# Performance work log

Hardware: AMD Instinct MI355X
Metric: run time of the kernel (lower is better)

## Reference

```python
import jax, jax.numpy as jnp
import numpy as np

H = 16
D_K = 64
D_V = 64


def setup_inputs() -> dict:
    key = jax.random.key(0)
    k0, k1, k2, k3, k4 = jax.random.split(key, 5)
    n, l, d_model = 4, 2048, 1024
    s = 1.0 / np.sqrt(d_model)
    Z = jax.random.normal(k0, (n, l, d_model), dtype=jnp.float32)
    mask = jnp.ones((n, 1, 1, l), dtype=jnp.int32)
    Wv = jax.random.normal(k1, (d_model, d_model), dtype=jnp.float32) * s
    Wk = jax.random.normal(k2, (d_model, H * D_K), dtype=jnp.float32) * s
    Wq = jax.random.normal(k3, (d_model, H * D_K), dtype=jnp.float32) * s
    Wo = jax.random.normal(k4, (H * D_V, d_model), dtype=jnp.float32) * s
    return {"Z": Z, "mask": mask, "Wv": Wv, "Wk": Wk, "Wq": Wq, "Wo": Wo}


def reference(Z, mask, Wv, Wk, Wq, Wo):
    n, l, d_model = Z.shape
    values = (Z @ Wv).reshape(n, l, H, D_V)
    keys = (Z @ Wk).reshape(n, l, H, D_K)
    queries = (Z @ Wq).reshape(n, l, H, D_K)
    # dense score matrix [n, h, q, k]
    C = jnp.einsum('nqhd,nkhd->nhqk', queries, keys)
    masked_C = jnp.where(mask == 0, -jnp.inf, C)
    idx = jnp.argmax(masked_C, axis=3)          # [n, h, q] hard top-1 index
    # torch einsum 'nhll,nlhd->nlhd' takes the diagonal of the one-hot
    # scattered C_tilde: diag element is C[n,h,l,l] iff argmax at query l is l.
    diag_C = jnp.einsum('nhll->nhl', C)         # [n, h, l]
    w = jnp.where(idx == jnp.arange(l)[None, None, :], diag_C, 0.0)  # [n, h, l]
    y_bar = (w.transpose(0, 2, 1)[..., None] * values).reshape(n, l, H * D_V)
    return y_bar @ Wo
```

## Files before the change

kernel.cpp:

```cpp
#include <hip/hip_runtime.h>
#include <hip/hip_bf16.h>
#include <string.h>

#define NB   4
#define LSEQ 2048
#define DMODEL 1024
#define NHEAD 16
#define DKH  64
#define CAND_CAP 32768

typedef __attribute__((ext_vector_type(8)))  short          short8v;
typedef __attribute__((ext_vector_type(8)))  unsigned short ushort8v;
typedef __attribute__((ext_vector_type(4)))  unsigned int   uint4v;
typedef __attribute__((ext_vector_type(16))) float          f32x16;

__device__ inline unsigned short bf16_rne(float v) {
  unsigned u = __builtin_bit_cast(unsigned, v);
  unsigned r = u + 0x7FFFu + ((u >> 16) & 1u);
  return (unsigned short)(r >> 16);
}
__device__ inline float bf16_to_f32(unsigned short u) {
  return __builtin_bit_cast(float, (unsigned)u << 16);
}
__device__ inline unsigned cvtpk2(float lo, float hi) {
  __hip_bfloat162 t = __float22bfloat162_rn(float2{lo, hi});
  unsigned u;
  memcpy(&u, &t, 4);
  return u;
}
__device__ inline void gload_lds16(const void* g, void* l) {
  __builtin_amdgcn_global_load_lds((const __attribute__((address_space(1))) void*)g,
                                   (__attribute__((address_space(3))) void*)l, 16, 0, 0);
}

__global__ __launch_bounds__(256) void zconv(
    const float* __restrict__ Z, unsigned short* __restrict__ Zbf) {
  size_t c = ((size_t)blockIdx.x * 256 + threadIdx.x) * 8;
  float4 a = *(const float4*)(Z + c), b = *(const float4*)(Z + c + 4);
  uint4v uv;
  uv[0] = cvtpk2(a.x, a.y);
  uv[1] = cvtpk2(a.z, a.w);
  uv[2] = cvtpk2(b.x, b.y);
  uv[3] = cvtpk2(b.z, b.w);
  *(ushort8v*)(Zbf + c) = __builtin_bit_cast(ushort8v, uv);
}

__global__ __launch_bounds__(256) void wconv(
    const float* __restrict__ Wq, const float* __restrict__ Wk,
    unsigned short* __restrict__ WThi) {
  __shared__ float T[64][65];
  const int col0 = blockIdx.x * 64, k0 = blockIdx.y * 64;
  const float* W = (col0 < 1024) ? Wq : Wk;
  const int cl0 = (col0 < 1024) ? col0 : col0 - 1024;
  const int tid = threadIdx.x;
#pragma unroll
  for (int u = 0; u < 16; ++u) {
    int lin = u * 256 + tid;
    int r = lin >> 6, c = lin & 63;
    T[r][c] = W[(size_t)(k0 + r) * 1024 + cl0 + c];
  }
  __syncthreads();
#pragma unroll
  for (int u = 0; u < 16; ++u) {
    int lin = u * 256 + tid;
    int cc = lin >> 6, kk = lin & 63;
    WThi[(size_t)(col0 + cc) * 1024 + k0 + kk] = bf16_rne(T[kk][cc]);
  }
}

__global__ __launch_bounds__(256) void proj_hi(
    const unsigned short* __restrict__ Zbf, const unsigned short* __restrict__ WThi,
    unsigned short* __restrict__ Qhd, unsigned short* __restrict__ Khd) {
  __shared__ unsigned short As[128 * 32];
  __shared__ unsigned short Bs[128 * 32];
  const int tid = threadIdx.x;
  const int lane = tid & 63, w = tid >> 6;
  const int l31 = lane & 31, half = lane >> 5;
  const int wrow = w >> 1, wcol = w & 1;
  const int bid = blockIdx.x;
  const int xcd = bid & 7, t = bid >> 3;
  const int brow = (xcd * 8 + (t & 7)) * 128;
  const int bcol = (t >> 3) * 128;

  int aoff[2], boff[2];
#pragma unroll
  for (int u = 0; u < 2; ++u) {
    int c = u * 256 + w * 64 + lane;
    int r = c >> 2, sp = c & 3;
    int s = sp ^ ((r >> 1) & 3);
    aoff[u] = (brow + r) * 1024 + s * 8;
    boff[u] = (bcol + r) * 1024 + s * 8;
  }

  f32x16 acc[2][2];
#pragma unroll
  for (int m = 0; m < 2; ++m)
#pragma unroll
    for (int nf = 0; nf < 2; ++nf)
#pragma unroll
      for (int r = 0; r < 16; ++r) acc[m][nf][r] = 0.f;

  for (int k0 = 0; k0 < 1024; k0 += 32) {
    __syncthreads();
#pragma unroll
    for (int u = 0; u < 2; ++u) {
      gload_lds16(Zbf  + (size_t)(aoff[u] + k0), (char*)As + u * 4096 + w * 1024);
      gload_lds16(WThi + (size_t)(boff[u] + k0), (char*)Bs + u * 4096 + w * 1024);
    }
    __syncthreads();
    short8v aH[2][2], bH[2][2];
#pragma unroll
    for (int m = 0; m < 2; ++m) {
      int r = wrow * 64 + m * 32 + l31;
      int sw = (r >> 1) & 3;
#pragma unroll
      for (int kc = 0; kc < 2; ++kc) {
        int sl = (kc * 2 + half) ^ sw;
        aH[m][kc] = *(const short8v*)((const char*)As + r * 64 + sl * 16);
      }
    }
#pragma unroll
    for (int nf = 0; nf < 2; ++nf) {
      int r = wcol * 64 + nf * 32 + l31;
      int sw = (r >> 1) & 3;
#pragma unroll
      for (int kc = 0; kc < 2; ++kc) {
        int sl = (kc * 2 + half) ^ sw;
        bH[nf][kc] = *(const short8v*)((const char*)Bs + r * 64 + sl * 16);
      }
    }
#pragma unroll
    for (int m = 0; m < 2; ++m)
#pragma unroll
      for (int nf = 0; nf < 2; ++nf)
#pragma unroll
        for (int kc = 0; kc < 2; ++kc)
          acc[m][nf] = __builtin_amdgcn_mfma_f32_32x32x16_bf16(aH[m][kc], bH[nf][kc], acc[m][nf], 0, 0, 0);
  }

  unsigned short* Out;
  int coff;
  if (bcol < 1024) { Out = Qhd; coff = bcol; } else { Out = Khd; coff = bcol - 1024; }
#pragma unroll
  for (int m = 0; m < 2; ++m)
#pragma unroll
    for (int nf = 0; nf < 2; ++nf) {
      int colg = coff + wcol * 64 + nf * 32 + l31;
      int head = colg >> 6, cin = colg & 63;
#pragma unroll
      for (int r = 0; r < 16; ++r) {
        int rowg = brow + wrow * 64 + m * 32 + (r & 3) + 8 * (r >> 2) + 4 * half;
        int n = rowg >> 11, l = rowg & 2047;
        Out[((size_t)(n * 16 + head) * 2048 + l) * 64 + cin] = bf16_rne(acc[m][nf][r]);
      }
    }
}

__global__ __launch_bounds__(256) void score_hi(
    const unsigned short* __restrict__ Qhd, const unsigned short* __restrict__ Khd,
    int* __restrict__ cnt_cand, int* __restrict__ cand) {
  __shared__ unsigned short Ks[64 * 128];
  const int tid = threadIdx.x;
  const int lane = tid & 63, w = tid >> 6;
  const int l31 = lane & 31, half = lane >> 5;
  const int bid = blockIdx.x;
  const int xcd = bid & 7, j = bid >> 3;
  const int nh = xcd + 8 * (j >> 4);
  const int qi = j & 15;
  const int n = nh >> 4, h = nh & 15;
  const int qw = qi * 128 + w * 32;

  const unsigned short* qrow = Qhd + ((size_t)(nh) * 2048 + qw + l31) * 64;
  short8v aQ[4];
#pragma unroll
  for (int ds = 0; ds < 4; ++ds)
    aQ[ds] = *(const short8v*)(qrow + ds * 16 + 8 * half);

  f32x16 zac;
#pragma unroll
  for (int r = 0; r < 16; ++r) zac[r] = 0.f;

  float maxO[16], diag[16];
#pragma unroll
  for (int r = 0; r < 16; ++r) { maxO[r] = -3.0e38f; diag[r] = -3.0e38f; }

  const unsigned short* kb = Khd + (size_t)nh * 2048 * 64;
  int koff[4];
#pragma unroll
  for (int u = 0; u < 4; ++u) {
    int c = u * 256 + w * 64 + lane;
    int pr = c >> 4, sp = c & 15;
    int ls = sp ^ (pr & 15);
    koff[u] = (2 * pr + (ls >> 3)) * 64 + (ls & 7) * 8;
  }

  for (int kt = 0; kt < LSEQ; kt += 128) {
    __syncthreads();
#pragma unroll
    for (int u = 0; u < 4; ++u)
      gload_lds16(kb + (size_t)kt * 64 + koff[u], (char*)Ks + u * 4096 + w * 1024);
    __syncthreads();
    char* buf = (char*)Ks;
    if (kt == qi * 128) {
#pragma unroll
      for (int ct = 0; ct < 4; ++ct) {
        const int rr = ct * 32 + l31;
        const int pr = rr >> 1;
        short8v bh[4];
#pragma unroll
        for (int ds = 0; ds < 4; ++ds) {
          int sl = ((rr & 1) << 3) | (2 * ds + half);
          bh[ds] = *(const short8v*)(buf + pr * 256 + ((sl ^ (pr & 15)) << 4));
        }
        f32x16 acc = __builtin_amdgcn_mfma_f32_32x32x16_bf16(aQ[0], bh[0], zac, 0, 0, 0);
#pragma unroll
        for (int ds = 1; ds < 4; ++ds)
          acc = __builtin_amdgcn_mfma_f32_32x32x16_bf16(aQ[ds], bh[ds], acc, 0, 0, 0);
        if (ct == w) {
#pragma unroll
          for (int r = 0; r < 16; ++r) {
            const int rloc = (r & 3) + 8 * (r >> 2) + 4 * half;
            if (l31 == rloc) diag[r] = acc[r];
            else             maxO[r] = fmaxf(maxO[r], acc[r]);
          }
        } else {
#pragma unroll
          for (int r = 0; r < 16; ++r) maxO[r] = fmaxf(maxO[r], acc[r]);
        }
      }
    } else {
#pragma unroll
      for (int p = 0; p < 2; ++p) {
        const int rrA = (2 * p) * 32 + l31, rrB = (2 * p + 1) * 32 + l31;
        const int prA = rrA >> 1, prB = rrB >> 1;
        short8v bA[4], bB[4];
#pragma unroll
        for (int ds = 0; ds < 4; ++ds) {
          int slA = ((rrA & 1) << 3) | (2 * ds + half);
          int slB = ((rrB & 1) << 3) | (2 * ds + half);
          bA[ds] = *(const short8v*)(buf + prA * 256 + ((slA ^ (prA & 15)) << 4));
          bB[ds] = *(const short8v*)(buf + prB * 256 + ((slB ^ (prB & 15)) << 4));
        }
        f32x16 accA = __builtin_amdgcn_mfma_f32_32x32x16_bf16(aQ[0], bA[0], zac, 0, 0, 0);
        f32x16 accB = __builtin_amdgcn_mfma_f32_32x32x16_bf16(aQ[0], bB[0], zac, 0, 0, 0);
#pragma unroll
        for (int ds = 1; ds < 4; ++ds) {
          accA = __builtin_amdgcn_mfma_f32_32x32x16_bf16(aQ[ds], bA[ds], accA, 0, 0, 0);
          accB = __builtin_amdgcn_mfma_f32_32x32x16_bf16(aQ[ds], bB[ds], accB, 0, 0, 0);
        }
#pragma unroll
        for (int r = 0; r < 16; ++r)
          maxO[r] = fmaxf(fmaxf(accA[r], accB[r]), maxO[r]);
      }
    }
  }

#pragma unroll
  for (int r = 0; r < 16; ++r) {
    float mo = maxO[r], dg = diag[r];
#pragma unroll
    for (int off = 16; off >= 1; off >>= 1) {
      mo = fmaxf(mo, __shfl_xor(mo, off));
      dg = fmaxf(dg, __shfl_xor(dg, off));
    }
    if (l31 == 0) {
      if (dg >= mo - 0.8f) {
        const int q = qw + (r & 3) + 8 * (r >> 2) + 4 * half;
        int slot = atomicAdd(cnt_cand, 1);
        if (slot < CAND_CAP) cand[slot] = (n << 15) | (h << 11) | q;
      }
    }
  }
}

__global__ __launch_bounds__(256) void recheck2(
    const float* __restrict__ Z, const float* __restrict__ Wq,
    const float* __restrict__ Wk, const float* __restrict__ Wv,
    const float* __restrict__ Wo, const unsigned short* __restrict__ Khd,
    const int* __restrict__ cnt_cand, const int* __restrict__ cand,
    float* __restrict__ out) {
  __shared__ float Zs[1024];
  __shared__ float part[4][64];
  __shared__ float Qex[64];
  __shared__ float Kex[64];
  __shared__ float Svals[2048];
  __shared__ float red[4];
  __shared__ int   Elist[64];
  __shared__ int   Ecnt;
  const int tid = threadIdx.x;
  const int lane = tid & 63, w = tid >> 6;
  int nc = *cnt_cand; if (nc > CAND_CAP) nc = CAND_CAP;

  for (int e = blockIdx.x; e < nc; e += gridDim.x) {
    const int pk = cand[e];
    const int n = pk >> 15, h = (pk >> 11) & 15, q = pk & 2047;
    __syncthreads();
#pragma unroll
    for (int u = 0; u < 4; ++u)
      Zs[tid + u * 256] = Z[((size_t)(n * LSEQ + q)) * 1024 + tid + u * 256];
    if (tid == 0) Ecnt = 0;
    __syncthreads();
    {
      int o = tid & 63, seg = tid >> 6;
      float p = 0.f;
      int d0 = seg * 256;
      for (int d = d0; d < d0 + 256; ++d) p += Zs[d] * Wq[(size_t)d * 1024 + h * 64 + o];
      part[seg][o] = p;
    }
    __syncthreads();
    if (tid < 64) Qex[tid] = part[0][tid] + part[1][tid] + part[2][tid] + part[3][tid];
    __syncthreads();
    const unsigned short* kb = Khd + (size_t)(n * 16 + h) * 2048 * 64;
    float mymax = -3.0e38f;
    for (int k = tid; k < LSEQ; k += 256) {
      const unsigned short* kr = kb + (size_t)k * 64;
      float s = 0.f;
#pragma unroll
      for (int jj = 0; jj < 8; ++jj) {
        ushort8v v = *(const ushort8v*)(kr + jj * 8);
#pragma unroll
        for (int ee = 0; ee < 8; ++ee) s += Qex[jj * 8 + ee] * bf16_to_f32(v[ee]);
      }
      Svals[k] = s;
      if (k != q) mymax = fmaxf(mymax, s);
    }
#pragma unroll
    for (int off = 32; off >= 1; off >>= 1) mymax = fmaxf(mymax, __shfl_xor(mymax, off));
    if (lane == 0) red[w] = mymax;
    __syncthreads();
    const float Mt = fmaxf(fmaxf(red[0], red[1]), fmaxf(red[2], red[3]));
    const float Sqt = Svals[q];
    if (Sqt < Mt - 0.4f) continue;
    for (int k = tid; k < LSEQ; k += 256) {
      if (k != q && Svals[k] >= Sqt - 0.4f) {
        int sl = atomicAdd(&Ecnt, 1);
        if (sl < 64) Elist[sl] = k;
      }
    }
    __syncthreads();
    const int nE = (Ecnt < 64) ? Ecnt : 64;
    float Sq_ex = 0.f;
    bool ok = true;
    for (int i = 0; i <= nE; ++i) {
      const int kk = (i == 0) ? q : Elist[i - 1];
      __syncthreads();
#pragma unroll
      for (int u = 0; u < 4; ++u)
        Zs[tid + u * 256] = Z[((size_t)(n * LSEQ + kk)) * 1024 + tid + u * 256];
      __syncthreads();
      {
        int o = tid & 63, seg = tid >> 6;
        float p = 0.f;
        int d0 = seg * 256;
        for (int d = d0; d < d0 + 256; ++d) p += Zs[d] * Wk[(size_t)d * 1024 + h * 64 + o];
        part[seg][o] = p;
      }
      __syncthreads();
      if (tid < 64) Kex[tid] = part[0][tid] + part[1][tid] + part[2][tid] + part[3][tid];
      __syncthreads();
      if (w == 0) {
        float pr = Qex[lane] * Kex[lane];
#pragma unroll
        for (int off = 32; off >= 1; off >>= 1) pr += __shfl_xor(pr, off);
        if (lane == 0) red[0] = pr;
      }
      __syncthreads();
      const float Sk = red[0];
      if (i == 0) Sq_ex = Sk;
      else        ok = ok && (kk < q ? (Sk < Sq_ex) : (Sk <= Sq_ex));
      __syncthreads();
    }
    if (!ok) continue;
    __syncthreads();
#pragma unroll
    for (int u = 0; u < 4; ++u)
      Zs[tid + u * 256] = Z[((size_t)(n * LSEQ + q)) * 1024 + tid + u * 256];
    __syncthreads();
    {
      int o = tid & 63, seg = tid >> 6;
      float p = 0.f;
      int d0 = seg * 256;
      for (int d = d0; d < d0 + 256; ++d) p += Zs[d] * Wv[(size_t)d * 1024 + h * 64 + o];
      part[seg][o] = p;
    }
    __syncthreads();
    if (tid < 64) Kex[tid] = part[0][tid] + part[1][tid] + part[2][tid] + part[3][tid];
    __syncthreads();
    {
      float a4[4] = {0.f, 0.f, 0.f, 0.f};
      const float* wo = Wo + (size_t)h * DKH * DMODEL;
      for (int jj = 0; jj < 64; ++jj) {
        float vj = Kex[jj];
#pragma unroll
        for (int u = 0; u < 4; ++u) a4[u] += vj * wo[(size_t)jj * DMODEL + tid + u * 256];
      }
      float* orow = out + ((size_t)n * LSEQ + q) * DMODEL;
#pragma unroll
      for (int u = 0; u < 4; ++u) atomicAdd(&orow[tid + u * 256], Sq_ex * a4[u]);
    }
  }
}

extern "C" void kernel_launch(void* const* d_in, const int* in_sizes, int n_in,
                              void* d_out, int out_size, void* d_ws, size_t ws_size,
                              hipStream_t stream) {
  const float* Z  = (const float*)d_in[0];
  const float* Wv = (const float*)d_in[2];
  const float* Wk = (const float*)d_in[3];
  const float* Wq = (const float*)d_in[4];
  const float* Wo = (const float*)d_in[5];
  float* out = (float*)d_out;

  int* cnt_cand = (int*)d_ws;
  int* cand = (int*)((char*)d_ws + 64);
  unsigned short* Khd  = (unsigned short*)((char*)d_ws + (size_t)(4 << 20));
  unsigned short* WThi = (unsigned short*)((char*)d_ws + (size_t)(24 << 20));
  unsigned short* Zbf  = (unsigned short*)((char*)d_ws + (size_t)(28 << 20));
  unsigned short* Qhd  = (unsigned short*)d_out;

  hipMemsetAsync(d_ws, 0, 64, stream);

  zconv<<<4096, 256, 0, stream>>>(Z, Zbf);

  dim3 gw(32, 16);
  wconv<<<gw, 256, 0, stream>>>(Wq, Wk, WThi);

  proj_hi<<<1024, 256, 0, stream>>>(Zbf, WThi, Qhd, Khd);

  score_hi<<<1024, 256, 0, stream>>>(Qhd, Khd, cnt_cand, cand);

  hipMemsetAsync(d_out, 0, (size_t)out_size * sizeof(float), stream);
  recheck2<<<256, 256, 0, stream>>>(Z, Wq, Wk, Wv, Wo, Khd, cnt_cand, cand, out);
}
```

Baseline: 186.4 us.

## Recheck scores via precomputed Wk·q vector instead of per-candidate key projections

In the exact recheck stage, the per-head query is folded into a 1024-wide vector u = Wk_h·q, computed once from a transposed fp32 copy of Wk. Each competing key's score then becomes a single dot product of its Z row with u, evaluated in parallel with one wave per candidate and an early exit on the first failure. Previously every competitor needed a full 1024x64 key projection in sequence. The change also adds a transpose kernel for Wk, splits the Q and V projections into four partial accumulators, doubles the recheck grid, and compacts the workspace layout. Associating the product differently can shift fp32 rounding in tie-sensitive comparisons.

```diff
diff --git a/kernel.cpp b/kernel.cpp
--- a/kernel.cpp
+++ b/kernel.cpp
@@ -65,6 +65,26 @@
     int lin = u * 256 + tid;
     int cc = lin >> 6, kk = lin & 63;
     WThi[(size_t)(col0 + cc) * 1024 + k0 + kk] = bf16_rne(T[kk][cc]);
+  }
+}
+
+__global__ __launch_bounds__(256) void wtr(
+    const float* __restrict__ Wk, float* __restrict__ WkT) {
+  __shared__ float T[64][65];
+  const int c0 = blockIdx.x * 64, d0 = blockIdx.y * 64;
+  const int tid = threadIdx.x;
+#pragma unroll
+  for (int u = 0; u < 16; ++u) {
+    int lin = u * 256 + tid;
+    int r = lin >> 6, c = lin & 63;
+    T[r][c] = Wk[(size_t)(d0 + r) * 1024 + c0 + c];
+  }
+  __syncthreads();
+#pragma unroll
+  for (int u = 0; u < 16; ++u) {
+    int lin = u * 256 + tid;
+    int cc = lin >> 6, dd = lin & 63;
+    WkT[(size_t)(c0 + cc) * 1024 + d0 + dd] = T[dd][cc];
   }
 }
 
@@ -273,22 +293,27 @@
   }
 }
 
-__global__ __launch_bounds__(256) void recheck2(
+__global__ __launch_bounds__(256) void recheck3(
     const float* __restrict__ Z, const float* __restrict__ Wq,
-    const float* __restrict__ Wk, const float* __restrict__ Wv,
-    const float* __restrict__ Wo, const unsigned short* __restrict__ Khd,
+    const float* __restrict__ Wv, const float* __restrict__ Wo,
+    const float* __restrict__ WkT, const unsigned short* __restrict__ Khd,
     const int* __restrict__ cnt_cand, const int* __restrict__ cand,
     float* __restrict__ out) {
   __shared__ float Zs[1024];
+  __shared__ float Us[1024];
   __shared__ float part[4][64];
   __shared__ float Qex[64];
   __shared__ float Kex[64];
   __shared__ float Svals[2048];
   __shared__ float red[4];
+  __shared__ float Sband[4];
+  __shared__ float SqS;
   __shared__ int   Elist[64];
   __shared__ int   Ecnt;
+  __shared__ int   okf;
   const int tid = threadIdx.x;
   const int lane = tid & 63, w = tid >> 6;
+  const int o = tid & 63, seg = tid >> 6;
   int nc = *cnt_cand; if (nc > CAND_CAP) nc = CAND_CAP;
 
   for (int e = blockIdx.x; e < nc; e += gridDim.x) {
@@ -298,17 +323,47 @@
 #pragma unroll
     for (int u = 0; u < 4; ++u)
       Zs[tid + u * 256] = Z[((size_t)(n * LSEQ + q)) * 1024 + tid + u * 256];
-    if (tid == 0) Ecnt = 0;
+    if (tid == 0) { Ecnt = 0; okf = 1; }
     __syncthreads();
     {
-      int o = tid & 63, seg = tid >> 6;
-      float p = 0.f;
+      const float* wc = Wq + h * 64 + o;
       int d0 = seg * 256;
-      for (int d = d0; d < d0 + 256; ++d) p += Zs[d] * Wq[(size_t)d * 1024 + h * 64 + o];
-      part[seg][o] = p;
+      float p0 = 0.f, p1 = 0.f, p2 = 0.f, p3 = 0.f;
+#pragma unroll
+      for (int d = 0; d < 256; d += 4) {
+        p0 += Zs[d0 + d]     * wc[(size_t)(d0 + d) * 1024];
+        p1 += Zs[d0 + d + 1] * wc[(size_t)(d0 + d + 1) * 1024];
+        p2 += Zs[d0 + d + 2] * wc[(size_t)(d0 + d + 2) * 1024];
+        p3 += Zs[d0 + d + 3] * wc[(size_t)(d0 + d + 3) * 1024];
+      }
+      part[seg][o] = (p0 + p1) + (p2 + p3);
     }
     __syncthreads();
     if (tid < 64) Qex[tid] = part[0][tid] + part[1][tid] + part[2][tid] + part[3][tid];
+    __syncthreads();
+    {
+      float u0 = 0.f, u1 = 0.f, u2 = 0.f, u3 = 0.f;
+      const float* base = WkT + (size_t)(h * 64) * 1024 + tid;
+      for (int c = 0; c < 64; ++c) {
+        float qc = Qex[c];
+        const float* col = base + (size_t)c * 1024;
+        u0 += qc * col[0];
+        u1 += qc * col[256];
+        u2 += qc * col[512];
+        u3 += qc * col[768];
+      }
+      Us[tid] = u0; Us[tid + 256] = u1; Us[tid + 512] = u2; Us[tid + 768] = u3;
+    }
+    __syncthreads();
+    {
+      float p = Zs[tid] * Us[tid] + Zs[tid + 256] * Us[tid + 256]
+              + Zs[tid + 512] * Us[tid + 512] + Zs[tid + 768] * Us[tid + 768];
+#pragma unroll
+      for (int off = 32; off >= 1; off >>= 1) p += __shfl_xor(p, off);
+      if (lane == 0) red[w] = p;
+    }
+    __syncthreads();
+    if (tid == 0) SqS = (red[0] + red[1]) + (red[2] + red[3]);
     __syncthreads();
     const unsigned short* kb = Khd + (size_t)(n * 16 + h) * 2048 * 64;
     float mymax = -3.0e38f;
@@ -339,49 +394,55 @@
     }
     __syncthreads();
     const int nE = (Ecnt < 64) ? Ecnt : 64;
-    float Sq_ex = 0.f;
-    bool ok = true;
-    for (int i = 0; i <= nE; ++i) {
-      const int kk = (i == 0) ? q : Elist[i - 1];
+    const float Sq_ex = SqS;
+    for (int i0 = 0; i0 < nE; i0 += 4) {
+      const int i = i0 + w;
+      float sk = 0.f;
+      if (i < nE) {
+        const int kk = Elist[i];
+        const float* zr = Z + ((size_t)(n * LSEQ + kk)) * 1024 + lane * 16;
+        float p0 = 0.f, p1 = 0.f;
+#pragma unroll
+        for (int jj = 0; jj < 16; jj += 8) {
+          float4 a = *(const float4*)(zr + jj);
+          float4 b = *(const float4*)(zr + jj + 4);
+          p0 += a.x * Us[lane * 16 + jj]     + a.y * Us[lane * 16 + jj + 1]
+              + a.z * Us[lane * 16 + jj + 2] + a.w * Us[lane * 16 + jj + 3];
+          p1 += b.x * Us[lane * 16 + jj + 4] + b.y * Us[lane * 16 + jj + 5]
+              + b.z * Us[lane * 16 + jj + 6] + b.w * Us[lane * 16 + jj + 7];
+        }
+        float p = p0 + p1;
+#pragma unroll
+        for (int off = 32; off >= 1; off >>= 1) p += __shfl_xor(p, off);
+        sk = p;
+      }
+      if (lane == 0) Sband[w] = sk;
       __syncthreads();
-#pragma unroll
-      for (int u = 0; u < 4; ++u)
-        Zs[tid + u * 256] = Z[((size_t)(n * LSEQ + kk)) * 1024 + tid + u * 256];
+      if (tid == 0) {
+        int okl = okf;
+        for (int ww = 0; ww < 4 && i0 + ww < nE; ++ww) {
+          int kk = Elist[i0 + ww];
+          float Sk = Sband[ww];
+          okl = okl && (kk < q ? (Sk < Sq_ex) : (Sk <= Sq_ex));
+        }
+        okf = okl;
+      }
       __syncthreads();
-      {
-        int o = tid & 63, seg = tid >> 6;
-        float p = 0.f;
-        int d0 = seg * 256;
-        for (int d = d0; d < d0 + 256; ++d) p += Zs[d] * Wk[(size_t)d * 1024 + h * 64 + o];
-        part[seg][o] = p;
-      }
-      __syncthreads();
-      if (tid < 64) Kex[tid] = part[0][tid] + part[1][tid] + part[2][tid] + part[3][tid];
-      __syncthreads();
-      if (w == 0) {
-        float pr = Qex[lane] * Kex[lane];
-#pragma unroll
-        for (int off = 32; off >= 1; off >>= 1) pr += __shfl_xor(pr, off);
-        if (lane == 0) red[0] = pr;
-      }
-      __syncthreads();
-      const float Sk = red[0];
-      if (i == 0) Sq_ex = Sk;
-      else        ok = ok && (kk < q ? (Sk < Sq_ex) : (Sk <= Sq_ex));
-      __syncthreads();
-    }
-    if (!ok) continue;
-    __syncthreads();
-#pragma unroll
-    for (int u = 0; u < 4; ++u)
-      Zs[tid + u * 256] = Z[((size_t)(n * LSEQ + q)) * 1024 + tid + u * 256];
-    __syncthreads();
+      if (!okf) break;
+    }
+    if (!okf) continue;
     {
-      int o = tid & 63, seg = tid >> 6;
-      float p = 0.f;
+      const float* wc = Wv + h * 64 + o;
       int d0 = seg * 256;
-      for (int d = d0; d < d0 + 256; ++d) p += Zs[d] * Wv[(size_t)d * 1024 + h * 64 + o];
-      part[seg][o] = p;
+      float p0 = 0.f, p1 = 0.f, p2 = 0.f, p3 = 0.f;
+#pragma unroll
+      for (int d = 0; d < 256; d += 4) {
+        p0 += Zs[d0 + d]     * wc[(size_t)(d0 + d) * 1024];
+        p1 += Zs[d0 + d + 1] * wc[(size_t)(d0 + d + 1) * 1024];
+        p2 += Zs[d0 + d + 2] * wc[(size_t)(d0 + d + 2) * 1024];
+        p3 += Zs[d0 + d + 3] * wc[(size_t)(d0 + d + 3) * 1024];
+      }
+      part[seg][o] = (p0 + p1) + (p2 + p3);
     }
     __syncthreads();
     if (tid < 64) Kex[tid] = part[0][tid] + part[1][tid] + part[2][tid] + part[3][tid];
@@ -413,9 +474,10 @@
 
   int* cnt_cand = (int*)d_ws;
   int* cand = (int*)((char*)d_ws + 64);
-  unsigned short* Khd  = (unsigned short*)((char*)d_ws + (size_t)(4 << 20));
-  unsigned short* WThi = (unsigned short*)((char*)d_ws + (size_t)(24 << 20));
-  unsigned short* Zbf  = (unsigned short*)((char*)d_ws + (size_t)(28 << 20));
+  float* WkT = (float*)((char*)d_ws + ((size_t)1 << 19));
+  unsigned short* WThi = (unsigned short*)((char*)d_ws + ((size_t)9 << 19));
+  unsigned short* Khd  = (unsigned short*)((char*)d_ws + ((size_t)17 << 19));
+  unsigned short* Zbf  = (unsigned short*)((char*)d_ws + ((size_t)49 << 19));
   unsigned short* Qhd  = (unsigned short*)d_out;
 
   hipMemsetAsync(d_ws, 0, 64, stream);
@@ -425,10 +487,13 @@
   dim3 gw(32, 16);
   wconv<<<gw, 256, 0, stream>>>(Wq, Wk, WThi);
 
+  dim3 gt(16, 16);
+  wtr<<<gt, 256, 0, stream>>>(Wk, WkT);
+
   proj_hi<<<1024, 256, 0, stream>>>(Zbf, WThi, Qhd, Khd);
 
   score_hi<<<1024, 256, 0, stream>>>(Qhd, Khd, cnt_cand, cand);
 
   hipMemsetAsync(d_out, 0, (size_t)out_size * sizeof(float), stream);
-  recheck2<<<256, 256, 0, stream>>>(Z, Wq, Wk, Wv, Wo, Khd, cnt_cand, cand, out);
-}
+  recheck3<<<512, 256, 0, stream>>>(Z, Wq, Wv, Wo, WkT, Khd, cnt_cand, cand, out);
+}
```

New measurement: 363.9 us. +95.3%, slower.
